# Kernel tuning notes

Measured on AMD Instinct MI355X. Metric: run time of the kernel, lower is better.

Reference implementation:

```python
import jax, jax.numpy as jnp
import numpy as np

DEG_CLAMP = 1e6  # matches .clamp(max=1000000.0) on deg^-0.5


def setup_inputs() -> dict:
    key = jax.random.key(0)
    k1, k2, k3 = jax.random.split(key, 3)
    N, E, D_IN, D_OUT = 100000, 1600000, 128, 128
    x = jax.random.normal(k1, (N, D_IN), dtype=jnp.float32)
    edge_index = jax.random.randint(k2, (2, E), 0, N, dtype=jnp.int64)
    # Linear params (xavier_uniform on weight, zero-ish bias)
    limit = float(np.sqrt(6.0 / (D_IN + D_OUT)))
    W = jax.random.uniform(k3, (D_OUT, D_IN), dtype=jnp.float32, minval=-limit, maxval=limit)
    b = jnp.zeros((D_OUT,), dtype=jnp.float32)
    return {"x": x, "edge_index": edge_index, "W": W, "b": b}


def reference(x, edge_index, W, b):
    N = x.shape[0]
    # append self-loops: ei = cat([edge_index, [arange(N); arange(N)]], dim=1)
    self_idx = jnp.arange(N, dtype=edge_index.dtype)
    src = jnp.concatenate([edge_index[0], self_idx])  # [E+N]
    dst = jnp.concatenate([edge_index[1], self_idx])  # [E+N]
    # degree of destination nodes (with self-loops)
    deg = jax.ops.segment_sum(jnp.ones_like(dst, dtype=x.dtype), dst, num_segments=N)
    deg_inv_sqrt = jnp.minimum(deg ** -0.5, DEG_CLAMP)
    # linear transform (dropout is identity in eval)
    h = x @ W.T + b  # [N, D_OUT]
    # symmetric normalization, gather, scale, scatter-add
    norm = deg_inv_sqrt[src] * deg_inv_sqrt[dst]  # [E+N]
    msgs = h[src] * norm[:, None]                  # [E+N, D_OUT]
    out = jax.ops.segment_sum(msgs, dst, num_segments=N)  # [N, D_OUT]
    return out
```

## Files before the change

### kernel.cpp

```cpp
#include <hip/hip_runtime.h>
#include <hip/hip_bf16.h>
#include <cstddef>

#define D 128
#define SHIFT 9
#define RN (1 << SHIFT)
#define CAPLOG 14
#define CAP (1 << CAPLOG)

typedef __attribute__((ext_vector_type(8))) short bf16x8;
typedef __attribute__((ext_vector_type(16))) float f32x16;

static __device__ __forceinline__ unsigned short f2bf(float f) {
  return __builtin_bit_cast(unsigned short, __float2bfloat16(f));
}

__global__ void k_initcur(int* __restrict__ gcursor, int nc) {
  int c = blockIdx.x * blockDim.x + threadIdx.x;
  if (c < nc) gcursor[c] = c << CAPLOG;
}

__global__ __launch_bounds__(256) void k_psort(
    const int* __restrict__ src, const int* __restrict__ dst,
    int* __restrict__ gcursor, unsigned* __restrict__ pairs, int e, int nc) {
  __shared__ int hist4[4][256];
  const int tid = threadIdx.x;
  const int w = tid >> 6;
  const int base = blockIdx.x * 4096;
  const int m = min(4096, e - base);
#pragma unroll
  for (int u = 0; u < 4; ++u) ((int*)hist4)[tid + 256 * u] = 0;
  __syncthreads();
  int myd[16], mys[16];
#pragma unroll
  for (int j = 0; j < 16; ++j) {
    const int i = tid + j * 256;
    if (i < m) {
      myd[j] = dst[base + i];
      mys[j] = src[base + i];
      atomicAdd(&hist4[w][myd[j] >> SHIFT], 1);
    }
  }
  __syncthreads();
  if (tid < nc) {
    const int t0 = hist4[0][tid], t1 = hist4[1][tid];
    const int t2 = hist4[2][tid], t3 = hist4[3][tid];
    const int tot = t0 + t1 + t2 + t3;
    int b = (tot > 0) ? atomicAdd(&gcursor[tid], tot) : 0;
    hist4[0][tid] = b;
    hist4[1][tid] = b + t0;
    hist4[2][tid] = b + t0 + t1;
    hist4[3][tid] = b + t0 + t1 + t2;
  }
  __syncthreads();
#pragma unroll
  for (int j = 0; j < 16; ++j) {
    const int i = tid + j * 256;
    if (i < m) {
      const int c = myd[j] >> SHIFT;
      const int pos = atomicAdd(&hist4[w][c], 1);
      const unsigned pk = (unsigned)mys[j] | ((unsigned)(myd[j] & (RN - 1)) << 22);
      __builtin_nontemporal_store(pk, &pairs[pos]);
    }
  }
}

__global__ __launch_bounds__(512) void k_fine(
    const unsigned* __restrict__ pairs, const int* __restrict__ gcursor,
    int* __restrict__ rowptr, int* __restrict__ cnt, float* __restrict__ dinv,
    int* __restrict__ srcs, int n) {
  __shared__ int hist[RN];
  __shared__ int rowL[RN];
  __shared__ int sdata[RN];
  const int c = blockIdx.x;
  const int tid = threadIdx.x;
  const int node0 = c << SHIFT;
  const int nodes = min(RN, n - node0);
  hist[tid] = 0;
  __syncthreads();
  const int beg = c << CAPLOG;
  const int end = gcursor[c];
  for (int i = beg + tid; i < end; i += RN)
    atomicAdd(&hist[pairs[i] >> 22], 1);
  __syncthreads();
  const int deg = hist[tid];
  const int p = (deg + 7) & ~7;
  sdata[tid] = p;
  __syncthreads();
  for (int off = 1; off < RN; off <<= 1) {
    int t = (tid >= off) ? sdata[tid - off] : 0;
    __syncthreads();
    sdata[tid] += t;
    __syncthreads();
  }
  const int rbase = beg + sdata[tid] - p;
  rowL[tid] = rbase;
  hist[tid] = rbase;
  if (tid < nodes) {
    rowptr[node0 + tid] = rbase;
    cnt[node0 + tid] = p;
    dinv[node0 + tid] = fminf(rsqrtf((float)(deg + 1)), 1.0e6f);
  }
  __syncthreads();
  for (int i = beg + tid; i < end; i += RN) {
    const unsigned pr = pairs[i];
    const int pos = atomicAdd(&hist[pr >> 22], 1);
    srcs[pos] = (int)(pr & 0x3FFFFFu);
  }
  __syncthreads();
  const int fend = rowL[tid] + p;
  for (int i = hist[tid]; i < fend; ++i) srcs[i] = n;
}

__global__ __launch_bounds__(256) void k_gemm(
    const float* __restrict__ x, const float* __restrict__ W,
    const float* __restrict__ bias, const float* __restrict__ dinv,
    __hip_bfloat16* __restrict__ g, int n) {
  __shared__ unsigned short xs[128 * 128];
  __shared__ unsigned short Ws[128 * 128];
  const int tid = threadIdx.x;
  const int row0 = blockIdx.x * 128;

#pragma unroll
  for (int u = 0; u < 8; ++u) {
    const int f = tid + 256 * u;
    const int row = f >> 4;
    const int c = f & 15;
    const int ch = (c ^ (row & 7)) << 3;
    {
      const float4* p = reinterpret_cast<const float4*>(&W[(size_t)row * D + c * 8]);
      const float4 v0 = p[0], v1 = p[1];
      uint4 pk;
      pk.x = f2bf(v0.x) | ((unsigned)f2bf(v0.y) << 16);
      pk.y = f2bf(v0.z) | ((unsigned)f2bf(v0.w) << 16);
      pk.z = f2bf(v1.x) | ((unsigned)f2bf(v1.y) << 16);
      pk.w = f2bf(v1.z) | ((unsigned)f2bf(v1.w) << 16);
      *reinterpret_cast<uint4*>(&Ws[row * 128 + ch]) = pk;
    }
    {
      float4 v0 = make_float4(0.f, 0.f, 0.f, 0.f), v1 = v0;
      if (row0 + row < n) {
        const float4* p =
            reinterpret_cast<const float4*>(&x[(size_t)(row0 + row) * D + c * 8]);
        v0 = p[0]; v1 = p[1];
      }
      uint4 pk;
      pk.x = f2bf(v0.x) | ((unsigned)f2bf(v0.y) << 16);
      pk.y = f2bf(v0.z) | ((unsigned)f2bf(v0.w) << 16);
      pk.z = f2bf(v1.x) | ((unsigned)f2bf(v1.y) << 16);
      pk.w = f2bf(v1.z) | ((unsigned)f2bf(v1.w) << 16);
      *reinterpret_cast<uint4*>(&xs[row * 128 + ch]) = pk;
    }
  }
  __syncthreads();

  const int lane = tid & 63;
  const int wv = tid >> 6;
  const int wr = (wv >> 1) * 64;
  const int wc = (wv & 1) * 64;
  const int lr = lane & 31;
  const int lk = lane >> 5;

  f32x16 acc[2][2];
#pragma unroll
  for (int m = 0; m < 2; ++m)
#pragma unroll
    for (int j = 0; j < 2; ++j)
#pragma unroll
      for (int q = 0; q < 16; ++q) acc[m][j][q] = 0.f;

#pragma unroll
  for (int ks = 0; ks < 8; ++ks) {
    bf16x8 a[2], b[2];
#pragma unroll
    for (int m = 0; m < 2; ++m) {
      const int r = wr + m * 32 + lr;
      const int ch = ((ks * 2 + lk) ^ (r & 7)) << 3;
      a[m] = *reinterpret_cast<const bf16x8*>(&xs[r * 128 + ch]);
    }
#pragma unroll
    for (int j = 0; j < 2; ++j) {
      const int r = wc + j * 32 + lr;
      const int ch = ((ks * 2 + lk) ^ (r & 7)) << 3;
      b[j] = *reinterpret_cast<const bf16x8*>(&Ws[r * 128 + ch]);
    }
#pragma unroll
    for (int m = 0; m < 2; ++m)
#pragma unroll
      for (int j = 0; j < 2; ++j)
        acc[m][j] = __builtin_amdgcn_mfma_f32_32x32x16_bf16(a[m], b[j], acc[m][j], 0, 0, 0);
  }

#pragma unroll
  for (int m = 0; m < 2; ++m) {
#pragma unroll
    for (int reg = 0; reg < 16; ++reg) {
      const int rloc = (reg & 3) + 8 * (reg >> 2) + 4 * lk;
      const int r = row0 + wr + m * 32 + rloc;
      if (r < n) {
        const float dv = dinv[r];
#pragma unroll
        for (int j = 0; j < 2; ++j) {
          const int col = wc + j * 32 + lr;
          g[(size_t)r * D + col] = __float2bfloat16((acc[m][j][reg] + bias[col]) * dv);
        }
      }
    }
  }
}

__global__ __launch_bounds__(256) void k_accum(
    const int* __restrict__ rowptr, const int* __restrict__ cnt,
    const int* __restrict__ srcs, const unsigned int* __restrict__ g2,
    const float* __restrict__ dinv, float2* __restrict__ out2, int n) {
  const int w = (int)(((size_t)blockIdx.x * 256 + threadIdx.x) >> 6);
  const int lane = threadIdx.x & 63;
  if (w >= n) return;
  const int beg = rowptr[w];
  const int num = cnt[w];
  const unsigned int v = g2[(size_t)w * 64 + lane];
  float ax = __uint_as_float(v << 16);
  float ay = __uint_as_float(v & 0xffff0000u);
  for (int k = 0; k < num; k += 8) {
    int s[8];
    unsigned int t[8];
#pragma unroll
    for (int u = 0; u < 8; ++u)
      s[u] = __builtin_nontemporal_load(&srcs[beg + k + u]);
#pragma unroll
    for (int u = 0; u < 8; ++u)
      t[u] = g2[(size_t)s[u] * 64 + lane];
#pragma unroll
    for (int u = 0; u < 8; ++u) {
      ax += __uint_as_float(t[u] << 16);
      ay += __uint_as_float(t[u] & 0xffff0000u);
    }
  }
  const float dv = dinv[w];
  const float2 res = make_float2(ax * dv, ay * dv);
  __builtin_nontemporal_store(__builtin_bit_cast(double, res),
                              (double*)(out2 + (size_t)w * 64 + lane));
}

extern "C" void kernel_launch(void* const* d_in, const int* in_sizes, int n_in,
                              void* d_out, int out_size, void* d_ws, size_t ws_size,
                              hipStream_t stream) {
  const float* x = (const float*)d_in[0];
  const int* ei = (const int*)d_in[1];
  const float* W = (const float*)d_in[2];
  const float* b = (const float*)d_in[3];
  float* out = (float*)d_out;
  const int n = in_sizes[0] / D;
  const int e = in_sizes[1] / 2;
  const int* src = ei;
  const int* dst = ei + e;
  const int nc = (n + RN - 1) >> SHIFT;

  char* ws = (char*)d_ws;
  const size_t nbb = ((size_t)n * 4 + 255) / 256 * 256;
  const size_t pb = (((size_t)nc << CAPLOG) * 4 + 255) / 256 * 256;
  float* dinv = (float*)ws;
  int* rowptr = (int*)(ws + nbb);
  int* cnt = (int*)(ws + 2 * nbb);
  int* gcursor = (int*)(ws + 3 * nbb);
  int* srcs = (int*)(ws + 3 * nbb + 1024);
  char* pr_base = ws + 3 * nbb + 1024 + pb;
  unsigned* pairs = (unsigned*)pr_base;
  __hip_bfloat16* g = (__hip_bfloat16*)pr_base;

  hipMemsetAsync(g + (size_t)n * D, 0, D * sizeof(__hip_bfloat16), stream);
  k_initcur<<<1, 256, 0, stream>>>(gcursor, nc);
  k_psort<<<(e + 4095) / 4096, 256, 0, stream>>>(src, dst, gcursor, pairs, e, nc);
  k_fine<<<nc, RN, 0, stream>>>(pairs, gcursor, rowptr, cnt, dinv, srcs, n);
  k_gemm<<<(n + 127) / 128, 256, 0, stream>>>(x, W, b, dinv, g, n);
  k_accum<<<(n + 3) / 4, 256, 0, stream>>>(rowptr, cnt, srcs, (const unsigned*)g,
                                           dinv, (float2*)out, n);
}
```

Before: 184.7 us.

## Split wavefront into half-waves gathering alternating neighbors with 8-byte loads

The accumulation kernel now has each half of a 64-lane wavefront gather a different neighbor row using 8-byte loads per lane. The two partial sums are combined with a cross-half shuffle, and the result is written as 16-byte stores. The next batch of source indices is prefetched while the current gathers run, and the memset plus cursor init are folded into one small kernel. This aims to double the number of independent row gathers in flight and remove one launch, at the cost of a shuffle reduction and idle stores in half the lanes.

```diff
diff --git a/kernel.cpp b/kernel.cpp
--- a/kernel.cpp
+++ b/kernel.cpp
@@ -10,14 +10,22 @@
 
 typedef __attribute__((ext_vector_type(8))) short bf16x8;
 typedef __attribute__((ext_vector_type(16))) float f32x16;
+typedef __attribute__((ext_vector_type(4))) float f32x4;
 
 static __device__ __forceinline__ unsigned short f2bf(float f) {
   return __builtin_bit_cast(unsigned short, __float2bfloat16(f));
 }
-
-__global__ void k_initcur(int* __restrict__ gcursor, int nc) {
-  int c = blockIdx.x * blockDim.x + threadIdx.x;
-  if (c < nc) gcursor[c] = c << CAPLOG;
+static __device__ __forceinline__ float bflo(unsigned u) {
+  return __uint_as_float(u << 16);
+}
+static __device__ __forceinline__ float bfhi(unsigned u) {
+  return __uint_as_float(u & 0xffff0000u);
+}
+
+__global__ void k_init(int* __restrict__ gcursor, int nc, unsigned* __restrict__ gz) {
+  const int t = threadIdx.x;
+  if (t < nc) gcursor[t] = t << CAPLOG;
+  if (t < 64) gz[t] = 0;
 }
 
 __global__ __launch_bounds__(256) void k_psort(
@@ -211,35 +219,54 @@
 
 __global__ __launch_bounds__(256) void k_accum(
     const int* __restrict__ rowptr, const int* __restrict__ cnt,
-    const int* __restrict__ srcs, const unsigned int* __restrict__ g2,
-    const float* __restrict__ dinv, float2* __restrict__ out2, int n) {
+    const int* __restrict__ srcs, const uint2* __restrict__ gq,
+    const float* __restrict__ dinv, float* __restrict__ out, int n) {
   const int w = (int)(((size_t)blockIdx.x * 256 + threadIdx.x) >> 6);
   const int lane = threadIdx.x & 63;
   if (w >= n) return;
+  const int li = lane & 31;
+  const int half = lane >> 5;
   const int beg = rowptr[w];
   const int num = cnt[w];
-  const unsigned int v = g2[(size_t)w * 64 + lane];
-  float ax = __uint_as_float(v << 16);
-  float ay = __uint_as_float(v & 0xffff0000u);
-  for (int k = 0; k < num; k += 8) {
-    int s[8];
-    unsigned int t[8];
-#pragma unroll
-    for (int u = 0; u < 8; ++u)
-      s[u] = __builtin_nontemporal_load(&srcs[beg + k + u]);
-#pragma unroll
-    for (int u = 0; u < 8; ++u)
-      t[u] = g2[(size_t)s[u] * 64 + lane];
-#pragma unroll
-    for (int u = 0; u < 8; ++u) {
-      ax += __uint_as_float(t[u] << 16);
-      ay += __uint_as_float(t[u] & 0xffff0000u);
-    }
-  }
-  const float dv = dinv[w];
-  const float2 res = make_float2(ax * dv, ay * dv);
-  __builtin_nontemporal_store(__builtin_bit_cast(double, res),
-                              (double*)(out2 + (size_t)w * 64 + lane));
+
+  const uint2 sv = gq[(size_t)(half ? n : w) * 32 + li];
+  float a0 = bflo(sv.x), a1 = bfhi(sv.x), a2 = bflo(sv.y), a3 = bfhi(sv.y);
+
+  if (num > 0) {
+    const int2* s2 = (const int2*)(srcs + beg);
+    int2 sp0 = s2[0], sp1 = s2[1], sp2 = s2[2], sp3 = s2[3];
+    for (int k = 0; k < num; k += 8) {
+      const int nxt = (k + 8 < num) ? (beg + k + 8) : beg;
+      const int2* s2n = (const int2*)(srcs + nxt);
+      const int2 np0 = s2n[0], np1 = s2n[1], np2 = s2n[2], np3 = s2n[3];
+      const int e0 = half ? sp0.y : sp0.x;
+      const int e1 = half ? sp1.y : sp1.x;
+      const int e2 = half ? sp2.y : sp2.x;
+      const int e3 = half ? sp3.y : sp3.x;
+      const uint2 t0 = gq[(size_t)e0 * 32 + li];
+      const uint2 t1 = gq[(size_t)e1 * 32 + li];
+      const uint2 t2 = gq[(size_t)e2 * 32 + li];
+      const uint2 t3 = gq[(size_t)e3 * 32 + li];
+      a0 += bflo(t0.x) + bflo(t1.x) + bflo(t2.x) + bflo(t3.x);
+      a1 += bfhi(t0.x) + bfhi(t1.x) + bfhi(t2.x) + bfhi(t3.x);
+      a2 += bflo(t0.y) + bflo(t1.y) + bflo(t2.y) + bflo(t3.y);
+      a3 += bfhi(t0.y) + bfhi(t1.y) + bfhi(t2.y) + bfhi(t3.y);
+      sp0 = np0; sp1 = np1; sp2 = np2; sp3 = np3;
+    }
+  }
+
+  a0 += __shfl_xor(a0, 32);
+  a1 += __shfl_xor(a1, 32);
+  a2 += __shfl_xor(a2, 32);
+  a3 += __shfl_xor(a3, 32);
+
+  if (!half) {
+    const float dv = dinv[w];
+    f32x4 res;
+    res[0] = a0 * dv; res[1] = a1 * dv; res[2] = a2 * dv; res[3] = a3 * dv;
+    f32x4* dst = (f32x4*)(out + (size_t)w * D) + li;
+    __builtin_nontemporal_store(res, dst);
+  }
 }
 
 extern "C" void kernel_launch(void* const* d_in, const int* in_sizes, int n_in,
@@ -268,11 +295,10 @@
   unsigned* pairs = (unsigned*)pr_base;
   __hip_bfloat16* g = (__hip_bfloat16*)pr_base;
 
-  hipMemsetAsync(g + (size_t)n * D, 0, D * sizeof(__hip_bfloat16), stream);
-  k_initcur<<<1, 256, 0, stream>>>(gcursor, nc);
+  k_init<<<1, 256, 0, stream>>>(gcursor, nc, (unsigned*)(g + (size_t)n * D));
   k_psort<<<(e + 4095) / 4096, 256, 0, stream>>>(src, dst, gcursor, pairs, e, nc);
   k_fine<<<nc, RN, 0, stream>>>(pairs, gcursor, rowptr, cnt, dinv, srcs, n);
   k_gemm<<<(n + 127) / 128, 256, 0, stream>>>(x, W, b, dinv, g, n);
-  k_accum<<<(n + 3) / 4, 256, 0, stream>>>(rowptr, cnt, srcs, (const unsigned*)g,
-                                           dinv, (float2*)out, n);
-}
+  k_accum<<<(n + 3) / 4, 256, 0, stream>>>(rowptr, cnt, srcs, (const uint2*)g,
+                                           dinv, out, n);
+}
```

Measured after the change: 179.5 us. 2.8% less time.
